# Kernel optimization log

Measured on AMD Instinct MI355X. Metric: run time of the kernel, lower is better.

The kernel has to match this reference:

```python
import jax, jax.numpy as jnp
import numpy as np
import math

B, N, E, H = 2, 2048, 1024, 16
D = E // H

def setup_inputs() -> dict:
    key = jax.random.key(0)
    ks = jax.random.split(key, 9)
    s = 1.0 / math.sqrt(E)
    return {
        "x": jax.random.normal(ks[0], (B, N, E), dtype=jnp.float32),
        "Wq": jax.random.uniform(ks[1], (E, E), jnp.float32, -s, s),
        "bq": jax.random.uniform(ks[2], (E,), jnp.float32, -s, s),
        "Wk": jax.random.uniform(ks[3], (E, E), jnp.float32, -s, s),
        "bk": jax.random.uniform(ks[4], (E,), jnp.float32, -s, s),
        "Wv": jax.random.uniform(ks[5], (E, E), jnp.float32, -s, s),
        "bv": jax.random.uniform(ks[6], (E,), jnp.float32, -s, s),
        "Wo": jax.random.uniform(ks[7], (E, E), jnp.float32, -s, s),
        "bo": jax.random.uniform(ks[8], (E,), jnp.float32, -s, s),
    }

def _split_heads(t):
    # [b, n, (h d)] -> [b, h, n, d]
    b, n, _ = t.shape
    return t.reshape(b, n, H, D).transpose(0, 2, 1, 3)

def reference(x, Wq, bq, Wk, bk, Wv, bv, Wo, bo):
    q = _split_heads(x @ Wq.T + bq)
    k = _split_heads(x @ Wk.T + bk)
    v = _split_heads(x @ Wv.T + bv)
    energy = jnp.einsum('bhqd,bhkd->bhqk', q, k)
    # Faithful to source: softmax first, THEN divide by sqrt(n_embedding)
    attention = jax.nn.softmax(energy, axis=-1) / jnp.sqrt(jnp.float32(E))
    out = jnp.einsum('bhqk,bhkd->bhqd', attention, v)
    out = out.transpose(0, 2, 1, 3).reshape(x.shape[0], x.shape[1], E)
    return out @ Wo.T + bo
```

## Files before the change

### kernel.cpp

```cpp
#include <hip/hip_runtime.h>


typedef __bf16 bf16x8 __attribute__((ext_vector_type(8)));
typedef float  f32x4  __attribute__((ext_vector_type(4)));
typedef float  f32x16 __attribute__((ext_vector_type(16)));
using u16 = unsigned short;
using u32 = unsigned int;
typedef u16 u16x8 __attribute__((ext_vector_type(8)));
typedef u16 u16x4 __attribute__((ext_vector_type(4)));
typedef u32 u32x4 __attribute__((ext_vector_type(4)));

constexpr int BATCH = 2, SEQ = 2048, EMB = 1024, NH = 16, HD = 64;
constexpr int MTOT = BATCH * SEQ;
constexpr int KTOT = EMB;
constexpr int NTOT = EMB;
constexpr float LOG2E = 1.44269504088896340736f;

constexpr size_t OFF_XBF = 0;
constexpr size_t OFF_WQ  = 8u * 1024 * 1024;
constexpr size_t OFF_WK  = OFF_WQ + 2u * 1024 * 1024;
constexpr size_t OFF_WV  = OFF_WK + 2u * 1024 * 1024;
constexpr size_t OFF_WO  = OFF_WV + 2u * 1024 * 1024;
constexpr size_t OFF_Q   = OFF_WO + 2u * 1024 * 1024;
constexpr size_t OFF_K   = OFF_Q  + 8u * 1024 * 1024;
constexpr size_t OFF_VT  = OFF_K  + 8u * 1024 * 1024;

__device__ __forceinline__ u16 f2bf(float f) {
  u32 u = __builtin_bit_cast(u32, f);
  u = (u + 0x7fffu + ((u >> 16) & 1u)) >> 16;
  return (u16)u;
}

__device__ __forceinline__ bf16x8 ld_bf16x8(const u16* p) {
  return __builtin_bit_cast(bf16x8, *(const u16x8*)p);
}

__device__ __forceinline__ float fexp2(float x) {
#if __has_builtin(__builtin_amdgcn_exp2f)
  return __builtin_amdgcn_exp2f(x);
#else
  return exp2f(x);
#endif
}

__device__ __forceinline__ float fmax3(float a, float b, float c) {
  float d;
  asm("v_max3_f32 %0, %1, %2, %3" : "=v"(d) : "v"(a), "v"(b), "v"(c));
  return d;
}

__device__ __forceinline__ u32 cvtpk(float lo, float hi_) {
  u32 r;
  asm("v_cvt_pk_bf16_f32 %0, %1, %2" : "=v"(r) : "v"(lo), "v"(hi_));
  return r;
}

__device__ __forceinline__ void stage16(const void* g, void* l) {
#if __has_builtin(__builtin_amdgcn_global_load_lds)
  __builtin_amdgcn_global_load_lds(
      (__attribute__((address_space(1))) void*)const_cast<void*>(g),
      (__attribute__((address_space(3))) void*)l, 16, 0, 0);
#else
  int lane = threadIdx.x & 63;
  uint4 v = *(const uint4*)g;
  *(uint4*)((char*)l + lane * 16) = v;
#endif
}

__global__ __launch_bounds__(256) void cvt_all(
    const float* __restrict__ x, const float* __restrict__ wq,
    const float* __restrict__ wk, const float* __restrict__ wv,
    const float* __restrict__ wo, u16* __restrict__ ox, u16* __restrict__ oq,
    u16* __restrict__ okk, u16* __restrict__ ov, u16* __restrict__ oo) {
  int z = blockIdx.z;
  const float* in = (z == 0) ? x : (z == 1) ? wq : (z == 2) ? wk : (z == 3) ? wv : wo;
  u16* out = (z == 0) ? ox : (z == 1) ? oq : (z == 2) ? okk : (z == 3) ? ov : oo;
  int n4 = (z == 0) ? (MTOT * EMB / 4) : (EMB * EMB / 4);
  int i = blockIdx.x * blockDim.x + threadIdx.x;
  if (i >= n4) return;
  float4 f = ((const float4*)in)[i];
  u32 lo = (u32)f2bf(f.x) | ((u32)f2bf(f.y) << 16);
  u32 hi = (u32)f2bf(f.z) | ((u32)f2bf(f.w) << 16);
  ((uint2*)out)[i] = make_uint2(lo, hi);
}

__device__ __forceinline__ void gemm_bt_core(const u16* __restrict__ A,
                                             const u16* __restrict__ Bm,
                                             const float* __restrict__ bias,
                                             void* __restrict__ out, int mode,
                                             float oscale) {
  __shared__ __align__(16) u16 sA[128 * 32];
  __shared__ __align__(16) u16 sB[128 * 32];
  const int tid = threadIdx.x, w = tid >> 6, ln = tid & 63;
  const int wr = w >> 1, wc = w & 1, qq = ln >> 4, t = ln & 15;
  const int m0 = blockIdx.y * 128, n0 = blockIdx.x * 128;

  f32x4 acc[4][4] = {};

  for (int kt = 0; kt < KTOT; kt += 32) {
#pragma unroll
    for (int j = 0; j < 2; j++) {
      int ck = w * 128 + j * 64 + ln;
      int r = ck >> 2, c2 = ck & 3;
      stage16(&A[(size_t)(m0 + r) * KTOT + kt + c2 * 8], &sA[(w * 128 + j * 64) * 8]);
      stage16(&Bm[(size_t)(n0 + r) * KTOT + kt + c2 * 8], &sB[(w * 128 + j * 64) * 8]);
    }
    __syncthreads();

    bf16x8 av[4], bv[4];
#pragma unroll
    for (int f = 0; f < 4; f++) {
      av[f] = ld_bf16x8(&sA[(wr * 64 + f * 16 + t) * 32 + qq * 8]);
      bv[f] = ld_bf16x8(&sB[(wc * 64 + f * 16 + t) * 32 + qq * 8]);
    }
    if (mode == 1) {
#pragma unroll
      for (int i = 0; i < 4; i++)
#pragma unroll
        for (int j = 0; j < 4; j++)
          acc[i][j] = __builtin_amdgcn_mfma_f32_16x16x32_bf16(bv[j], av[i], acc[i][j], 0, 0, 0);
    } else {
#pragma unroll
      for (int i = 0; i < 4; i++)
#pragma unroll
        for (int j = 0; j < 4; j++)
          acc[i][j] = __builtin_amdgcn_mfma_f32_16x16x32_bf16(av[i], bv[j], acc[i][j], 0, 0, 0);
    }
    __syncthreads();
  }

  if (mode == 1) {
#pragma unroll
    for (int j = 0; j < 4; j++)
#pragma unroll
      for (int ii = 0; ii < 4; ii++) {
        int n = n0 + wc * 64 + j * 16 + qq * 4 + ii;
        float bn = bias[n];
        int h = n >> 6, d = n & 63;
#pragma unroll
        for (int i = 0; i < 4; i++) {
          int mm = m0 + wr * 64 + i * 16 + t;
          int b = mm >> 11, tok = mm & 2047;
          ((u16*)out)[(((size_t)(b * NH + h)) * HD + d) * SEQ + tok] =
              f2bf(acc[i][j][ii] + bn);
        }
      }
    return;
  }

#pragma unroll
  for (int fc = 0; fc < 4; fc++) {
    int n = n0 + wc * 64 + fc * 16 + t;
    float bn = bias[n];
#pragma unroll
    for (int fr = 0; fr < 4; fr++) {
#pragma unroll
      for (int i = 0; i < 4; i++) {
        int m = m0 + wr * 64 + fr * 16 + qq * 4 + i;
        float v = (acc[fr][fc][i] + bn) * oscale;
        if (mode == 2) {
          ((float*)out)[(size_t)m * NTOT + n] = v;
        } else {
          int b = m >> 11, tok = m & 2047, h = n >> 6, d = n & 63;
          ((u16*)out)[(((size_t)(b * NH + h)) * SEQ + tok) * HD + d] = f2bf(v);
        }
      }
    }
  }
}

__global__ __launch_bounds__(256) void gemm_qkv(
    const u16* __restrict__ A, const u16* __restrict__ WQ, const u16* __restrict__ WK,
    const u16* __restrict__ WV, const float* __restrict__ bq, const float* __restrict__ bk,
    const float* __restrict__ bv, u16* Qo, u16* Ko, u16* Vo) {
  int z = blockIdx.z;
  const u16* Bm = (z == 0) ? WQ : ((z == 1) ? WK : WV);
  const float* bias = (z == 0) ? bq : ((z == 1) ? bk : bv);
  u16* out = (z == 0) ? Qo : ((z == 1) ? Ko : Vo);
  gemm_bt_core(A, Bm, bias, out, (z == 2) ? 1 : 0, (z == 0) ? LOG2E : 1.0f);
}

__global__ __launch_bounds__(256) void gemm_o(const u16* __restrict__ A,
                                              const u16* __restrict__ WO,
                                              const float* __restrict__ bo,
                                              float* __restrict__ out) {
  gemm_bt_core(A, WO, bo, out, 2, 1.0f);
}

__global__ __launch_bounds__(512, 4) void flash_attn(const u16* __restrict__ Q,
                                                     const u16* __restrict__ Kg,
                                                     const u16* __restrict__ VT,
                                                     u16* __restrict__ O) {
  const int e = blockIdx.x;
  const int xcd = e & 7, slot = e >> 3;
  const int bh = xcd * 4 + (slot & 3);
  const int qt = slot >> 2;

  const int tid = threadIdx.x, w = tid >> 6, ln = tid & 63;
  const int c = ln & 31, hi = ln >> 5;
  const int kb = w >> 2;
  const int q0 = qt * 128 + (w & 3) * 32;

  const u16* Qb = Q + (size_t)bh * SEQ * HD;
  const u16* Kb = Kg + (size_t)bh * SEQ * HD;
  const u16* Vb = VT + (size_t)bh * HD * SEQ;

  __shared__ __align__(16) u16 sK[2][64 * 64];
  __shared__ __align__(16) u16 sV[2][64 * 64];
  __shared__ float2 sml[8][64];

  bf16x8 qf[4];
#pragma unroll
  for (int ks = 0; ks < 4; ks++)
    qf[ks] = ld_bf16x8(&Qb[(size_t)(q0 + c) * HD + ks * 16 + hi * 8]);

  const bf16x8 ones = __builtin_bit_cast(
      bf16x8, (u16x8){0x3f80, 0x3f80, 0x3f80, 0x3f80, 0x3f80, 0x3f80, 0x3f80, 0x3f80});

  f32x16 ot[2];
  ot[0] = 0.f; ot[1] = 0.f;
  f32x16 acc_l = 0.f;
  float m = -1e30f;

#define STAGE(buf, kt)                                                         \
  {                                                                            \
    int ck = w * 64 + ln;                                                      \
    int r = ck >> 3, c2 = ck & 7, c2s = c2 ^ (r & 7);                          \
    stage16(&Kb[(size_t)((kt) + r) * HD + c2s * 8],                            \
            &sK[buf][(size_t)(w * 64) * 8]);                                   \
    stage16(&Vb[(size_t)r * SEQ + (kt) + c2s * 8],                             \
            &sV[buf][(size_t)(w * 64) * 8]);                                   \
  }

  STAGE(0, 0)
  __syncthreads();

  int it = 0;
  for (int kt = 0; kt < SEQ; kt += 64, it ^= 1) {
    if (kt + 64 < SEQ) STAGE(it ^ 1, kt + 64)
    const u16* kbuf = sK[it];
    const u16* vbuf = sV[it];

    f32x16 st = 0.f;
    __builtin_amdgcn_s_setprio(1);
#pragma unroll
    for (int ks = 0; ks < 4; ks++) {
      int row = kb * 32 + c;
      int boff = ((2 * ks + hi) ^ (row & 7)) << 4;
      bf16x8 kf = ld_bf16x8((const u16*)((const char*)(kbuf + row * 64) + boff));
      st = __builtin_amdgcn_mfma_f32_32x32x16_bf16(kf, qf[ks], st, 0, 0, 0);
    }
    __builtin_amdgcn_s_setprio(0);

    float a0 = fmax3(st[0], st[1], st[2]);
    float a1 = fmax3(st[3], st[4], st[5]);
    float a2 = fmax3(st[6], st[7], st[8]);
    float a3 = fmax3(st[9], st[10], st[11]);
    float a4 = fmax3(st[12], st[13], st[14]);
    float a5 = fmaxf(st[15], a0);
    float b0 = fmax3(a1, a2, a3);
    float b1 = fmax3(a4, a5, b0);
    float pmax = fmaxf(b1, __shfl_xor(b1, 32));

    if (!__all(pmax <= m + 8.0f)) {
      float mn = fmaxf(m, pmax);
      float sc = fexp2(m - mn);
      acc_l[0] *= sc;
#pragma unroll
      for (int i = 0; i < 16; i++) { ot[0][i] *= sc; ot[1][i] *= sc; }
      m = mn;
    }

#pragma unroll
    for (int i = 0; i < 16; i++) st[i] = fexp2(st[i] - m);

    bf16x8 pb[2];
#pragma unroll
    for (int ks2 = 0; ks2 < 2; ks2++) {
      const int R0 = 8 * ks2;
      const int R1 = 4 * ((2 * ks2 + 1) & 3);
      u32 X0 = cvtpk(st[R0], st[R0 + 1]);
      u32 X1 = cvtpk(st[R0 + 2], st[R0 + 3]);
      u32 Y0 = cvtpk(st[R1], st[R1 + 1]);
      u32 Y1 = cvtpk(st[R1 + 2], st[R1 + 3]);
      asm("v_permlane32_swap_b32 %0, %1" : "+v"(X0), "+v"(Y0));
      asm("v_permlane32_swap_b32 %0, %1" : "+v"(X1), "+v"(Y1));
      u32x4 wd; wd.x = X0; wd.y = X1; wd.z = Y0; wd.w = Y1;
      pb[ks2] = __builtin_bit_cast(bf16x8, wd);
    }

    __builtin_amdgcn_s_setprio(1);
#pragma unroll
    for (int ks2 = 0; ks2 < 2; ks2++) {
#pragma unroll
      for (int db = 0; db < 2; db++) {
        int row = db * 32 + c;
        int boff = ((kb * 4 + ks2 * 2 + hi) ^ (row & 7)) << 4;
        bf16x8 vf = ld_bf16x8((const u16*)((const char*)(vbuf + row * 64) + boff));
        ot[db] = __builtin_amdgcn_mfma_f32_32x32x16_bf16(vf, pb[ks2], ot[db], 0, 0, 0);
      }
      acc_l = __builtin_amdgcn_mfma_f32_32x32x16_bf16(ones, pb[ks2], acc_l, 0, 0, 0);
    }
    __builtin_amdgcn_s_setprio(0);
    __syncthreads();
  }
#undef STAGE

  float myl = acc_l[0];
  const int pair = w & 3;
  float* xA = (float*)sK;
  float* xB = (float*)sV;
  {
    f32x16 give = (w < 4) ? ot[1] : ot[0];
    *(f32x16*)((w < 4 ? xA : xB) + (size_t)(pair * 64 + ln) * 16) = give;
    sml[w][ln] = make_float2(m, myl);
  }
  __syncthreads();

  float2 po = sml[w ^ 4][ln];
  float M2 = fmaxf(m, po.x);
  float s_me = fexp2(m - M2), s_po = fexp2(po.x - M2);
  float lf = myl * s_me + po.y * s_po;
  float inv = 1.0f / (lf * 32.0f);
  f32x16 oth = *(const f32x16*)((w < 4 ? xB : xA) + (size_t)(pair * 64 + ln) * 16);
  f32x16 own = (w < 4) ? ot[0] : ot[1];
  const int db = (w < 4) ? 0 : 1;

  const int b = bh >> 4, h = bh & 15;
  u16* obase = O + ((size_t)(b * SEQ + q0 + c)) * EMB + h * HD;
#pragma unroll
  for (int g = 0; g < 4; g++) {
    u16x4 pkt;
#pragma unroll
    for (int i = 0; i < 4; i++)
      pkt[i] = f2bf((own[g * 4 + i] * s_me + oth[g * 4 + i] * s_po) * inv);
    *(u16x4*)(obase + db * 32 + g * 8 + hi * 4) = pkt;
  }
}

extern "C" void kernel_launch(void* const* d_in, const int* in_sizes, int n_in,
                              void* d_out, int out_size, void* d_ws, size_t ws_size,
                              hipStream_t stream) {
  const float* x  = (const float*)d_in[0];
  const float* Wq = (const float*)d_in[1];
  const float* bq = (const float*)d_in[2];
  const float* Wk = (const float*)d_in[3];
  const float* bk = (const float*)d_in[4];
  const float* Wv = (const float*)d_in[5];
  const float* bv = (const float*)d_in[6];
  const float* Wo = (const float*)d_in[7];
  const float* bo = (const float*)d_in[8];

  char* ws = (char*)d_ws;
  u16* xbf = (u16*)(ws + OFF_XBF);
  u16* wqb = (u16*)(ws + OFF_WQ);
  u16* wkb = (u16*)(ws + OFF_WK);
  u16* wvb = (u16*)(ws + OFF_WV);
  u16* wob = (u16*)(ws + OFF_WO);
  u16* Qw  = (u16*)(ws + OFF_Q);
  u16* Kw  = (u16*)(ws + OFF_K);
  u16* Vw  = (u16*)(ws + OFF_VT);

  cvt_all<<<dim3(MTOT * EMB / 4 / 256, 1, 5), 256, 0, stream>>>(
      x, Wq, Wk, Wv, Wo, xbf, wqb, wkb, wvb, wob);

  gemm_qkv<<<dim3(NTOT / 128, MTOT / 128, 3), 256, 0, stream>>>(
      xbf, wqb, wkb, wvb, bq, bk, bv, Qw, Kw, Vw);

  flash_attn<<<dim3(512), 512, 0, stream>>>(Qw, Kw, Vw, xbf);

  gemm_o<<<dim3(NTOT / 128, MTOT / 128), 256, 0, stream>>>(xbf, wob, bo, (float*)d_out);
}
```

Measured before the change: 135.0 us.

## Split QKV GEMM by mode and halve flash-attention block to 64 queries

Templates the GEMM core on output mode so the per-block mode branches resolve at compile time, and splits the fused QKV launch into a Q/K launch plus a separate V-transpose launch. The flash-attention kernel now uses 256 threads covering 64 query rows per block, with 1024 blocks instead of 512, and each wave stages two chunks of K/V. The aim is finer-grained scheduling and less runtime branching, at the cost of an extra kernel launch and twice as many K/V tile loads per query row across blocks.

```diff
diff --git a/kernel.cpp b/kernel.cpp
--- a/kernel.cpp
+++ b/kernel.cpp
@@ -84,10 +84,11 @@
   ((uint2*)out)[i] = make_uint2(lo, hi);
 }
 
+template <int MODE>
 __device__ __forceinline__ void gemm_bt_core(const u16* __restrict__ A,
                                              const u16* __restrict__ Bm,
                                              const float* __restrict__ bias,
-                                             void* __restrict__ out, int mode,
+                                             void* __restrict__ out,
                                              float oscale) {
   __shared__ __align__(16) u16 sA[128 * 32];
   __shared__ __align__(16) u16 sB[128 * 32];
@@ -113,23 +114,19 @@
       av[f] = ld_bf16x8(&sA[(wr * 64 + f * 16 + t) * 32 + qq * 8]);
       bv[f] = ld_bf16x8(&sB[(wc * 64 + f * 16 + t) * 32 + qq * 8]);
     }
-    if (mode == 1) {
-#pragma unroll
-      for (int i = 0; i < 4; i++)
-#pragma unroll
-        for (int j = 0; j < 4; j++)
+#pragma unroll
+    for (int i = 0; i < 4; i++)
+#pragma unroll
+      for (int j = 0; j < 4; j++) {
+        if (MODE == 1)
           acc[i][j] = __builtin_amdgcn_mfma_f32_16x16x32_bf16(bv[j], av[i], acc[i][j], 0, 0, 0);
-    } else {
-#pragma unroll
-      for (int i = 0; i < 4; i++)
-#pragma unroll
-        for (int j = 0; j < 4; j++)
+        else
           acc[i][j] = __builtin_amdgcn_mfma_f32_16x16x32_bf16(av[i], bv[j], acc[i][j], 0, 0, 0);
-    }
+      }
     __syncthreads();
   }
 
-  if (mode == 1) {
+  if (MODE == 1) {
 #pragma unroll
     for (int j = 0; j < 4; j++)
 #pragma unroll
@@ -158,7 +155,7 @@
       for (int i = 0; i < 4; i++) {
         int m = m0 + wr * 64 + fr * 16 + qq * 4 + i;
         float v = (acc[fr][fc][i] + bn) * oscale;
-        if (mode == 2) {
+        if (MODE == 2) {
           ((float*)out)[(size_t)m * NTOT + n] = v;
         } else {
           int b = m >> 11, tok = m & 2047, h = n >> 6, d = n & 63;
@@ -169,25 +166,30 @@
   }
 }
 
-__global__ __launch_bounds__(256) void gemm_qkv(
+__global__ __launch_bounds__(256) void gemm_qk(
     const u16* __restrict__ A, const u16* __restrict__ WQ, const u16* __restrict__ WK,
-    const u16* __restrict__ WV, const float* __restrict__ bq, const float* __restrict__ bk,
-    const float* __restrict__ bv, u16* Qo, u16* Ko, u16* Vo) {
-  int z = blockIdx.z;
-  const u16* Bm = (z == 0) ? WQ : ((z == 1) ? WK : WV);
-  const float* bias = (z == 0) ? bq : ((z == 1) ? bk : bv);
-  u16* out = (z == 0) ? Qo : ((z == 1) ? Ko : Vo);
-  gemm_bt_core(A, Bm, bias, out, (z == 2) ? 1 : 0, (z == 0) ? LOG2E : 1.0f);
+    const float* __restrict__ bq, const float* __restrict__ bk, u16* Qo, u16* Ko) {
+  if (blockIdx.z == 0)
+    gemm_bt_core<0>(A, WQ, bq, Qo, LOG2E);
+  else
+    gemm_bt_core<0>(A, WK, bk, Ko, 1.0f);
+}
+
+__global__ __launch_bounds__(256) void gemm_vt(const u16* __restrict__ A,
+                                               const u16* __restrict__ WV,
+                                               const float* __restrict__ bv,
+                                               u16* Vo) {
+  gemm_bt_core<1>(A, WV, bv, Vo, 1.0f);
 }
 
 __global__ __launch_bounds__(256) void gemm_o(const u16* __restrict__ A,
                                               const u16* __restrict__ WO,
                                               const float* __restrict__ bo,
                                               float* __restrict__ out) {
-  gemm_bt_core(A, WO, bo, out, 2, 1.0f);
-}
-
-__global__ __launch_bounds__(512, 4) void flash_attn(const u16* __restrict__ Q,
+  gemm_bt_core<2>(A, WO, bo, out, 1.0f);
+}
+
+__global__ __launch_bounds__(256, 4) void flash_attn(const u16* __restrict__ Q,
                                                      const u16* __restrict__ Kg,
                                                      const u16* __restrict__ VT,
                                                      u16* __restrict__ O) {
@@ -198,8 +200,8 @@
 
   const int tid = threadIdx.x, w = tid >> 6, ln = tid & 63;
   const int c = ln & 31, hi = ln >> 5;
-  const int kb = w >> 2;
-  const int q0 = qt * 128 + (w & 3) * 32;
+  const int kb = w >> 1;
+  const int q0 = qt * 64 + (w & 1) * 32;
 
   const u16* Qb = Q + (size_t)bh * SEQ * HD;
   const u16* Kb = Kg + (size_t)bh * SEQ * HD;
@@ -207,7 +209,7 @@
 
   __shared__ __align__(16) u16 sK[2][64 * 64];
   __shared__ __align__(16) u16 sV[2][64 * 64];
-  __shared__ float2 sml[8][64];
+  __shared__ float2 sml[4][64];
 
   bf16x8 qf[4];
 #pragma unroll
@@ -224,12 +226,14 @@
 
 #define STAGE(buf, kt)                                                         \
   {                                                                            \
-    int ck = w * 64 + ln;                                                      \
-    int r = ck >> 3, c2 = ck & 7, c2s = c2 ^ (r & 7);                          \
-    stage16(&Kb[(size_t)((kt) + r) * HD + c2s * 8],                            \
-            &sK[buf][(size_t)(w * 64) * 8]);                                   \
-    stage16(&Vb[(size_t)r * SEQ + (kt) + c2s * 8],                             \
-            &sV[buf][(size_t)(w * 64) * 8]);                                   \
+    _Pragma("unroll") for (int j = 0; j < 2; j++) {                            \
+      int ck = w * 128 + j * 64 + ln;                                          \
+      int r = ck >> 3, c2 = ck & 7, c2s = c2 ^ (r & 7);                        \
+      stage16(&Kb[(size_t)((kt) + r) * HD + c2s * 8],                          \
+              &sK[buf][(size_t)(w * 128 + j * 64) * 8]);                       \
+      stage16(&Vb[(size_t)r * SEQ + (kt) + c2s * 8],                           \
+              &sV[buf][(size_t)(w * 128 + j * 64) * 8]);                       \
+    }                                                                          \
   }
 
   STAGE(0, 0)
@@ -307,24 +311,24 @@
 #undef STAGE
 
   float myl = acc_l[0];
-  const int pair = w & 3;
+  const int pair = w & 1;
   float* xA = (float*)sK;
   float* xB = (float*)sV;
   {
-    f32x16 give = (w < 4) ? ot[1] : ot[0];
-    *(f32x16*)((w < 4 ? xA : xB) + (size_t)(pair * 64 + ln) * 16) = give;
+    f32x16 give = (kb == 0) ? ot[1] : ot[0];
+    *(f32x16*)((kb == 0 ? xA : xB) + (size_t)(pair * 64 + ln) * 16) = give;
     sml[w][ln] = make_float2(m, myl);
   }
   __syncthreads();
 
-  float2 po = sml[w ^ 4][ln];
+  float2 po = sml[w ^ 2][ln];
   float M2 = fmaxf(m, po.x);
   float s_me = fexp2(m - M2), s_po = fexp2(po.x - M2);
   float lf = myl * s_me + po.y * s_po;
   float inv = 1.0f / (lf * 32.0f);
-  f32x16 oth = *(const f32x16*)((w < 4 ? xB : xA) + (size_t)(pair * 64 + ln) * 16);
-  f32x16 own = (w < 4) ? ot[0] : ot[1];
-  const int db = (w < 4) ? 0 : 1;
+  f32x16 oth = *(const f32x16*)((kb == 0 ? xB : xA) + (size_t)(pair * 64 + ln) * 16);
+  f32x16 own = (kb == 0) ? ot[0] : ot[1];
+  const int db = kb;
 
   const int b = bh >> 4, h = bh & 15;
   u16* obase = O + ((size_t)(b * SEQ + q0 + c)) * EMB + h * HD;
@@ -364,10 +368,11 @@
   cvt_all<<<dim3(MTOT * EMB / 4 / 256, 1, 5), 256, 0, stream>>>(
       x, Wq, Wk, Wv, Wo, xbf, wqb, wkb, wvb, wob);
 
-  gemm_qkv<<<dim3(NTOT / 128, MTOT / 128, 3), 256, 0, stream>>>(
-      xbf, wqb, wkb, wvb, bq, bk, bv, Qw, Kw, Vw);
-
-  flash_attn<<<dim3(512), 512, 0, stream>>>(Qw, Kw, Vw, xbf);
+  gemm_qk<<<dim3(NTOT / 128, MTOT / 128, 2), 256, 0, stream>>>(
+      xbf, wqb, wkb, bq, bk, Qw, Kw);
+  gemm_vt<<<dim3(NTOT / 128, MTOT / 128), 256, 0, stream>>>(xbf, wvb, bv, Vw);
+
+  flash_attn<<<dim3(1024), 256, 0, stream>>>(Qw, Kw, Vw, xbf);
 
   gemm_o<<<dim3(NTOT / 128, MTOT / 128), 256, 0, stream>>>(xbf, wob, bo, (float*)d_out);
 }
```

After: 141.8 us. 5.0% more time.
